# Kernel tuning notes

Measured on AMD Instinct MI355X. Metric: run time of the kernel, lower is better.

The kernel has to match this reference:

```python
import jax, jax.numpy as jnp
import numpy as np

N_NODE = 10000
E = 320000
E_LINK = 1280000
D = 128            # emb_input_dim = n_factors*delta_d = hid_dim
EDGE_FEAT = 24     # 2 + ceil(64/3)
SEQ = 64
K = 3


def _propagate(x, src, dst, w, n_seg):
    # out[d] = sum_{e: dst[e]=d} w[e] * x[src[e]]  (sparse matvec via gather-scatter)
    return jax.ops.segment_sum(w[:, None] * x[src], dst, num_segments=n_seg)


def setup_inputs() -> dict:
    key = jax.random.key(0)
    ks = jax.random.split(key, 16)
    inp = {
        "h_entity": jax.random.normal(ks[0], (SEQ, N_NODE, D), dtype=jnp.float32),
        "x_link": jax.random.normal(ks[1], (E, EDGE_FEAT), dtype=jnp.float32),
        "edge_weight_link": jax.random.uniform(ks[2], (E_LINK,), dtype=jnp.float32),
        "edge_index_link": jax.random.randint(ks[3], (2, E_LINK), 0, E, dtype=jnp.int32),
        "edge_index": jax.random.randint(ks[4], (2, E), 0, N_NODE, dtype=jnp.int32),
    }
    s = 0.05
    inp.update({
        "W_start": jax.random.normal(ks[5], (EDGE_FEAT, D), dtype=jnp.float32) * s,
        "b_start": jnp.zeros((D,), jnp.float32),
        "W_hl": jax.random.normal(ks[6], (K, D, D), dtype=jnp.float32) * s,
        "b_hl": jnp.zeros((D,), jnp.float32),
        "W_ec": jax.random.normal(ks[7], (D, K * 2), dtype=jnp.float32) * s,
        "b_ec": jnp.zeros((K * 2,), jnp.float32),
        "W_t": jax.random.normal(ks[8], (SEQ, 1), dtype=jnp.float32) * s,
        "b_t": jnp.zeros((1,), jnp.float32),
        "W_gcn": jax.random.normal(ks[9], (K, D, D), dtype=jnp.float32) * s,
        "b_gcn": jnp.zeros((D,), jnp.float32),
    })
    return inp


def reference(h_entity, x_link, edge_weight_link, W_start, b_start, W_hl, b_hl,
              W_ec, b_ec, W_t, b_t, W_gcn, b_gcn, edge_index_link, edge_index):
    src_l, dst_l = edge_index_link[0], edge_index_link[1]
    src_n, dst_n = edge_index[0], edge_index[1]

    # start_mlp_edge
    h_link = x_link @ W_start + b_start                      # [E, D]

    # HodgeLaguerreConv, K=3: Laguerre polynomial recurrence on edge Laplacian L
    # Tx0 = x; Tx1 = (1 - L)x; Tx_{k+1} = ((2k+1-L)Tx_k - k Tx_{k-1})/(k+1)
    Tx0 = h_link
    out_e = Tx0 @ W_hl[0]
    Tx1 = Tx0 - _propagate(Tx0, src_l, dst_l, edge_weight_link, E)
    out_e = out_e + Tx1 @ W_hl[1]
    Tx2 = (3.0 * Tx1 - _propagate(Tx1, src_l, dst_l, edge_weight_link, E) - Tx0) * 0.5
    out_e = out_e + Tx2 @ W_hl[2] + b_hl                     # [E, D]

    # per-edge causal scores, K*2 columns
    score = out_e @ W_ec + b_ec                              # [E, 2K]

    # temporal projection: [T,N,D] -> permute -> [N,D,T] @ [T,1] -> [N,D]
    h_ent = jnp.einsum('tnd,t->nd', h_entity, W_t[:, 0]) + b_t[0]

    # K-hop GCN: hop-k edge weight = softmax over the (causal, non-causal) pair k
    w_k = jax.nn.softmax(score.reshape(E, K, 2), axis=-1)[..., 0]  # [E, K]
    h = h_ent
    out_n = jnp.zeros((N_NODE, D), dtype=h_ent.dtype)
    for k in range(K):
        h = _propagate(h, src_n, dst_n, w_k[:, k], N_NODE)
        out_n = out_n + h @ W_gcn[k]
    out_n = out_n + b_gcn
    return out_n
```

## Files before the change

### kernel.cpp

```cpp
#include <hip/hip_runtime.h>

#define N_NODE   10000
#define E_EDGE   320000
#define E_LINKN  1280000
#define DIM      128
#define EFEAT    24
#define SEQLEN   64

#define SCAN_CHUNK 4096
#define NB_L 79
#define NB_N 3

static const size_t OFF_DEGN  = 0;
static const size_t OFF_DEGL  = OFF_DEGN  + 10240*4;
static const size_t OFF_DONE  = OFF_DEGL  + (size_t)E_EDGE*4;
static const size_t ZERO_BYTES= OFF_DONE  + 256;
static const size_t OFF_CONST = ZERO_BYTES;
static const size_t OFF_V0    = OFF_CONST + 512*4;
static const size_t OFF_V12   = OFF_V0    + (size_t)E_EDGE*6*4;
static const size_t OFF_PW    = OFF_V12   + (size_t)E_EDGE*16*4;
static const size_t OFF_STARTN= OFF_PW    + (size_t)E_EDGE*16*4;
static const size_t OFF_SRCSN = OFF_STARTN+ 10304*4;
static const size_t OFF_POSN  = OFF_SRCSN + (size_t)E_EDGE*4;
static const size_t OFF_WKS4  = OFF_POSN  + (size_t)E_EDGE*4;
static const size_t OFF_STARTL= OFF_WKS4  + (size_t)E_EDGE*16;
static const size_t OFF_LSW   = OFF_STARTL+ ((size_t)E_EDGE+64)*4;
static const size_t OFF_HENT  = OFF_LSW   + (size_t)E_LINKN*8;
static const size_t OFF_HA    = OFF_HENT  + (size_t)N_NODE*DIM*4;
static const size_t OFF_HB    = OFF_HA    + (size_t)N_NODE*DIM*4;
static const size_t OFF_HC    = OFF_HB    + (size_t)N_NODE*DIM*4;
static const size_t OFF_PARTN = OFF_HC    + (size_t)N_NODE*DIM*4;
static const size_t OFF_PARTL = OFF_PARTN + 512*4;

__global__ void consts_kernel(const float* __restrict__ Wstart, const float* __restrict__ bstart,
                              const float* __restrict__ Whl,    const float* __restrict__ bhl,
                              const float* __restrict__ Wec,    const float* __restrict__ bec,
                              float* __restrict__ Ball, float* __restrict__ cvec,
                              int4* __restrict__ zreg) {
    __shared__ float M[128*129];
    __shared__ float sWec[768];
    __shared__ float A[768];
    int k = blockIdx.x;
    int t = threadIdx.x;

    for (int i = blockIdx.x*256 + t; i < (int)(ZERO_BYTES/16); i += 3*256)
        zreg[i] = make_int4(0, 0, 0, 0);

    for (int i = t; i < 768; i += 256) sWec[i] = Wec[i];

    const float* w0 = Whl;
    const float* w1 = Whl + 16384;
    const float* w2 = Whl + 32768;
    for (int idx = t; idx < 16384; idx += 256) {
        int r = idx >> 7, d = idx & 127;
        float m;
        if (k == 0)      m = w0[idx] + w1[idx] + w2[idx];
        else if (k == 1) m = -(w1[idx] + 2.f*w2[idx]);
        else             m = 0.5f * w2[idx];
        M[r*129 + d] = m;
    }
    __syncthreads();

    for (int idx = t; idx < 768; idx += 256) {
        int r = idx / 6, j = idx % 6;
        float s = 0.f;
        for (int d = 0; d < 128; d++) s += M[r*129 + d] * sWec[d*6 + j];
        A[idx] = s;
    }
    __syncthreads();

    if (t < 144) {
        int i = t / 6, j = t % 6;
        float s = 0.f;
        for (int r = 0; r < 128; r++) s += Wstart[i*128 + r] * A[r*6 + j];
        Ball[i*18 + k*6 + j] = s;
    } else if (t < 150) {
        int j = t - 144;
        float s = 0.f;
        for (int r = 0; r < 128; r++) s += bstart[r] * A[r*6 + j];
        cvec[k*6 + j] = s;
    } else if (k == 0 && t >= 160 && t < 166) {
        int j = t - 160;
        float s = bec[j];
        for (int d = 0; d < 128; d++) s += bhl[d] * sWec[d*6 + j];
        cvec[18 + j] = s;
    }
}

__global__ void v_hist_kernel(const float* __restrict__ x, const float* __restrict__ Ball,
                              const int* __restrict__ dstl, const int* __restrict__ dstn,
                              float* __restrict__ V0, float* __restrict__ V12,
                              int* __restrict__ degl, int* __restrict__ degn) {
    int e = blockIdx.x * 256 + threadIdx.x;
    atomicAdd(degl + dstl[e], 1);

    if (blockIdx.x >= 1250) return;
    atomicAdd(degn + dstn[e], 1);

    __shared__ float sB[432];
    for (int i = threadIdx.x; i < 432; i += 256) sB[i] = Ball[i];
    __syncthreads();

    float xr[24];
    const float4* xp = (const float4*)(x + (size_t)e*24);
#pragma unroll
    for (int q = 0; q < 6; q++) {
        float4 v = xp[q];
        xr[4*q+0] = v.x; xr[4*q+1] = v.y; xr[4*q+2] = v.z; xr[4*q+3] = v.w;
    }
    float o[18];
#pragma unroll
    for (int j = 0; j < 18; j++) o[j] = 0.f;
#pragma unroll
    for (int i = 0; i < 24; i++) {
        float xv = xr[i];
#pragma unroll
        for (int j = 0; j < 18; j++) o[j] += xv * sB[i*18 + j];
    }
    float2* v0p = (float2*)(V0 + (size_t)e*6);
    v0p[0] = make_float2(o[0], o[1]);
    v0p[1] = make_float2(o[2], o[3]);
    v0p[2] = make_float2(o[4], o[5]);
    float4* v12p = (float4*)(V12 + (size_t)e*16);
    v12p[0] = make_float4(o[6],  o[7],  o[8],  o[9]);
    v12p[1] = make_float4(o[10], o[11], o[12], o[13]);
    v12p[2] = make_float4(o[14], o[15], o[16], o[17]);
}

__global__ void partial_scanp_kernel(const int* __restrict__ degl, const int* __restrict__ degn,
                                     int* __restrict__ partl, int* __restrict__ partn,
                                     int* __restrict__ done,
                                     int* __restrict__ startl, int* __restrict__ startn) {
    __shared__ int red[256];
    __shared__ int lastflag;
    int b = blockIdx.x, t = threadIdx.x;

    const int* deg; int n, base; int* part;
    if (b < NB_L) { deg = degl; n = E_EDGE;  base = b*SCAN_CHUNK;          part = partl + b; }
    else          { deg = degn; n = N_NODE;  base = (b-NB_L)*SCAN_CHUNK;   part = partn + (b-NB_L); }

    int s = 0;
    for (int i = t; i < SCAN_CHUNK; i += 256) {
        int idx = base + i;
        if (idx < n) s += deg[idx];
    }
    red[t] = s;
    __syncthreads();
    for (int off = 128; off > 0; off >>= 1) {
        if (t < off) red[t] += red[t + off];
        __syncthreads();
    }
    if (t == 0) {
        *part = red[0];
        __threadfence();
        lastflag = (atomicAdd(done, 1) == NB_L + NB_N - 1);
    }
    __syncthreads();
    if (!lastflag) return;
    __threadfence();

    {
        __shared__ int a[256];
        a[t] = (t < NB_L) ? partl[t] : 0;
        __syncthreads();
        for (int off = 1; off < 256; off <<= 1) {
            int v = (t >= off) ? a[t - off] : 0;
            __syncthreads();
            a[t] += v;
            __syncthreads();
        }
        partl[256 + t] = (t == 0) ? 0 : a[t - 1];
        if (t == 255) startl[E_EDGE] = a[NB_L - 1];
    }
    __syncthreads();
    {
        __shared__ int a2[256];
        a2[t] = (t < NB_N) ? partn[t] : 0;
        __syncthreads();
        for (int off = 1; off < 256; off <<= 1) {
            int v = (t >= off) ? a2[t - off] : 0;
            __syncthreads();
            a2[t] += v;
            __syncthreads();
        }
        partn[256 + t] = (t == 0) ? 0 : a2[t - 1];
        if (t == 255) startn[N_NODE] = a2[NB_N - 1];
    }
}

__global__ void scan_block_kernel(const int* __restrict__ degl, const int* __restrict__ degn,
                                  const int* __restrict__ partl, const int* __restrict__ partn,
                                  int* __restrict__ startl, int* __restrict__ startn) {
    __shared__ int s[SCAN_CHUNK];
    __shared__ int tsum[256];
    int b = blockIdx.x, t = threadIdx.x;

    const int* deg; const int* offs; int* start; int n, base;
    if (b < NB_L) { deg = degl; offs = partl + 256; start = startl; n = E_EDGE; base = b*SCAN_CHUNK; }
    else { deg = degn; offs = partn + 256; start = startn; n = N_NODE; base = (b-NB_L)*SCAN_CHUNK; b -= NB_L; }

    for (int i = t; i < SCAN_CHUNK; i += 256) {
        int idx = base + i;
        s[i] = (idx < n) ? deg[idx] : 0;
    }
    __syncthreads();
    int lo = t * 16;
    int mysum = 0;
#pragma unroll
    for (int j = 0; j < 16; j++) mysum += s[lo + j];
    tsum[t] = mysum;
    __syncthreads();
    for (int off = 1; off < 256; off <<= 1) {
        int v = (t >= off) ? tsum[t - off] : 0;
        __syncthreads();
        tsum[t] += v;
        __syncthreads();
    }
    int run = offs[b] + ((t == 0) ? 0 : tsum[t - 1]);
#pragma unroll
    for (int j = 0; j < 16; j++) {
        int v = s[lo + j];
        s[lo + j] = run;
        run += v;
    }
    __syncthreads();
    for (int i = t; i < SCAN_CHUNK; i += 256) {
        int idx = base + i;
        if (idx < n) start[idx] = s[i];
    }
}

__global__ void fill_both_kernel(const int* __restrict__ srcl, const int* __restrict__ dstl,
                                 const float* __restrict__ ewl,
                                 const int* __restrict__ srcn, const int* __restrict__ dstn,
                                 const int* __restrict__ startl, const int* __restrict__ startn,
                                 int* __restrict__ degl, int* __restrict__ degn,
                                 int2* __restrict__ lsw,
                                 int* __restrict__ srcs_srt, int* __restrict__ posn) {
    int e = blockIdx.x * 256 + threadIdx.x;
    {
        int d = dstl[e];
        int old = atomicSub(degl + d, 1);
        int p = startl[d] + old - 1;
        lsw[p] = make_int2(srcl[e], __float_as_int(ewl[e]));
    }
    if (blockIdx.x < 1250) {
        int d = dstn[e];
        int old = atomicSub(degn + d, 1);
        int p = startn[d] + old - 1;
        srcs_srt[p] = srcn[e];
        posn[e] = p;
    }
}

__global__ void prop1_gather(const float* __restrict__ V12, const int* __restrict__ startl,
                             const int2* __restrict__ lsw, float* __restrict__ PW) {
    int e = blockIdx.x * blockDim.x + threadIdx.x;
    if (e >= E_EDGE) return;
    int s0 = startl[e], s1 = startl[e + 1];
    float acc[12];
#pragma unroll
    for (int j = 0; j < 12; j++) acc[j] = 0.f;
    float ws = 0.f;
    int2 cur = make_int2(0, 0);
    if (s0 < s1) cur = lsw[s0];
    for (int j = s0; j < s1; j++) {
        int2 nxt = (j + 1 < s1) ? lsw[j + 1] : cur;
        float w = __int_as_float(cur.y);
        const float4* vp = (const float4*)(V12 + (size_t)cur.x*16);
#pragma unroll
        for (int q = 0; q < 3; q++) {
            float4 v = vp[q];
            acc[4*q+0] += w*v.x; acc[4*q+1] += w*v.y;
            acc[4*q+2] += w*v.z; acc[4*q+3] += w*v.w;
        }
        ws += w;
        cur = nxt;
    }
    float4* pw = (float4*)(PW + (size_t)e*16);
    pw[0] = make_float4(acc[0], acc[1], acc[2],  acc[3]);
    pw[1] = make_float4(acc[4], acc[5], acc[6],  acc[7]);
    pw[2] = make_float4(acc[8], acc[9], acc[10], acc[11]);
    pw[3] = make_float4(ws, 0.f, 0.f, 0.f);
}

__global__ void prop2score_kernel(const float* __restrict__ PW,
                                  const int* __restrict__ startl, const int2* __restrict__ lsw,
                                  const float* __restrict__ V0,
                                  const float* __restrict__ cvec, const int* __restrict__ posn,
                                  float4* __restrict__ wks4) {
    __shared__ float sc[24];
    if (threadIdx.x < 24) sc[threadIdx.x] = cvec[threadIdx.x];
    __syncthreads();
    int e = blockIdx.x * blockDim.x + threadIdx.x;
    if (e >= E_EDGE) return;
    int s0 = startl[e], s1 = startl[e + 1];
    float p2[6];
#pragma unroll
    for (int j = 0; j < 6; j++) p2[j] = 0.f;
    float ws2 = 0.f;
    int2 cur = make_int2(0, 0);
    if (s0 < s1) cur = lsw[s0];
    for (int j = s0; j < s1; j++) {
        int2 nxt = (j + 1 < s1) ? lsw[j + 1] : cur;
        float w = __int_as_float(cur.y);
        const float4* pv = (const float4*)(PW + (size_t)cur.x*16);
        float4 a = pv[1];
        float4 b = pv[2];
        float4 c = pv[3];
        p2[0] += w*a.z; p2[1] += w*a.w;
        p2[2] += w*b.x; p2[3] += w*b.y; p2[4] += w*b.z; p2[5] += w*b.w;
        ws2 += w * c.x;
        cur = nxt;
    }
    const float4* pe = (const float4*)(PW + (size_t)e*16);
    float4 q0 = pe[0];
    float4 q1 = pe[1];
    float  ws1 = pe[3].x;
    float pw6[6] = {q0.x, q0.y, q0.z, q0.w, q1.x, q1.y};
    const float2* v0p = (const float2*)(V0 + (size_t)e*6);
    float2 f0 = v0p[0], f1 = v0p[1], f2 = v0p[2];
    float v0r[6] = {f0.x, f0.y, f1.x, f1.y, f2.x, f2.y};
    float S[6];
#pragma unroll
    for (int j = 0; j < 6; j++)
        S[j] = v0r[j] + pw6[j] + p2[j]
             + ws1*sc[6 + j] + ws2*sc[12 + j] + sc[j] + sc[18 + j];
    int p = posn[e];
    float w0 = 1.f / (1.f + __expf(S[1] - S[0]));
    float w1 = 1.f / (1.f + __expf(S[3] - S[2]));
    float w2 = 1.f / (1.f + __expf(S[5] - S[4]));
    wks4[p] = make_float4(w0, w1, w2, 0.f);
}

__global__ void temporal_kernel(const float4* __restrict__ h_entity, const float* __restrict__ Wt,
                                const float* __restrict__ bt, float4* __restrict__ h_ent) {
    __shared__ float sw[SEQLEN];
    if (threadIdx.x < SEQLEN) sw[threadIdx.x] = Wt[threadIdx.x];
    __syncthreads();
    int i = blockIdx.x * blockDim.x + threadIdx.x;
    if (i >= N_NODE*DIM/4) return;
    float b = bt[0];
    float4 acc = make_float4(b, b, b, b);
#pragma unroll 8
    for (int t = 0; t < SEQLEN; t++) {
        float4 v = h_entity[(size_t)t * (N_NODE*DIM/4) + i];
        float w = sw[t];
        acc.x += w*v.x; acc.y += w*v.y; acc.z += w*v.z; acc.w += w*v.w;
    }
    h_ent[i] = acc;
}

__global__ void prop_hop(const float* __restrict__ h_cur, float* __restrict__ h_next,
                         const int* __restrict__ startn, const int* __restrict__ srcs_srt,
                         const float4* __restrict__ wks4, int k) {
    int half = threadIdx.x >> 7;
    int tid  = threadIdx.x & 127;
    int node = blockIdx.x * 2 + half;
    int s0 = startn[node], s1 = startn[node + 1];
    float acc = 0.f;
    int sn = 0; float w = 0.f;
    if (s0 < s1) {
        sn = srcs_srt[s0];
        float4 wv = wks4[s0];
        w = (k == 0) ? wv.x : (k == 1) ? wv.y : wv.z;
    }
    for (int j = s0; j < s1; j++) {
        int sn_c = sn; float w_c = w;
        if (j + 1 < s1) {
            sn = srcs_srt[j + 1];
            float4 wv = wks4[j + 1];
            w = (k == 0) ? wv.x : (k == 1) ? wv.y : wv.z;
        }
        acc += w_c * h_cur[(size_t)sn_c*DIM + tid];
    }
    h_next[(size_t)node*DIM + tid] = acc;
}

__global__ void __launch_bounds__(256)
gemm_final(const float* __restrict__ h1, const float* __restrict__ h2,
           const float* __restrict__ h3, const float* __restrict__ Wgcn,
           const float* __restrict__ bgcn, float* __restrict__ out) {
    __shared__ float sG[128*128];
    __shared__ float sh[32*128];
    int t = threadIdx.x;
    int cg = t & 31, rg = t >> 5;
    int c0 = cg * 4, r0 = rg * 4;
    int rbase = blockIdx.x * 32;
    int nrows = N_NODE - rbase; if (nrows > 32) nrows = 32;

    float4 bb = *(const float4*)(bgcn + c0);
    float acc[4][4];
#pragma unroll
    for (int r = 0; r < 4; r++) {
        acc[r][0] = bb.x; acc[r][1] = bb.y; acc[r][2] = bb.z; acc[r][3] = bb.w;
    }

    const float* hs0[3] = {h1, h2, h3};
    for (int k = 0; k < 3; k++) {
        __syncthreads();
        const float4* gk = (const float4*)(Wgcn + (size_t)k*16384);
        float4* sg4 = (float4*)sG;
        for (int i = t; i < 4096; i += 256) sg4[i] = gk[i];
        const float4* hg = (const float4*)(hs0[k] + (size_t)rbase*128);
        float4* sh4 = (float4*)sh;
        for (int i = t; i < 1024; i += 256)
            sh4[i] = ((i >> 5) < nrows) ? hg[i] : make_float4(0.f, 0.f, 0.f, 0.f);
        __syncthreads();
#pragma unroll 2
        for (int d4 = 0; d4 < 32; d4++) {
            float4 g0 = *(const float4*)(sG + (d4*4 + 0)*128 + c0);
            float4 g1 = *(const float4*)(sG + (d4*4 + 1)*128 + c0);
            float4 g2 = *(const float4*)(sG + (d4*4 + 2)*128 + c0);
            float4 g3 = *(const float4*)(sG + (d4*4 + 3)*128 + c0);
#pragma unroll
            for (int r = 0; r < 4; r++) {
                float4 hv = *(const float4*)(sh + (r0 + r)*128 + d4*4);
                acc[r][0] += hv.x*g0.x; acc[r][1] += hv.x*g0.y; acc[r][2] += hv.x*g0.z; acc[r][3] += hv.x*g0.w;
                acc[r][0] += hv.y*g1.x; acc[r][1] += hv.y*g1.y; acc[r][2] += hv.y*g1.z; acc[r][3] += hv.y*g1.w;
                acc[r][0] += hv.z*g2.x; acc[r][1] += hv.z*g2.y; acc[r][2] += hv.z*g2.z; acc[r][3] += hv.z*g2.w;
                acc[r][0] += hv.w*g3.x; acc[r][1] += hv.w*g3.y; acc[r][2] += hv.w*g3.z; acc[r][3] += hv.w*g3.w;
            }
        }
    }
#pragma unroll
    for (int r = 0; r < 4; r++) {
        if (r0 + r < nrows)
            *(float4*)(out + (size_t)(rbase + r0 + r)*128 + c0) =
                make_float4(acc[r][0], acc[r][1], acc[r][2], acc[r][3]);
    }
}

extern "C" void kernel_launch(void* const* d_in, const int* in_sizes, int n_in,
                              void* d_out, int out_size, void* d_ws, size_t ws_size,
                              hipStream_t stream) {
    const float* h_entity = (const float*)d_in[0];
    const float* x_link   = (const float*)d_in[1];
    const float* ewl      = (const float*)d_in[2];
    const int*   eil      = (const int*)d_in[3];
    const int*   ein      = (const int*)d_in[4];
    const float* Wstart   = (const float*)d_in[5];
    const float* bstart   = (const float*)d_in[6];
    const float* Whl      = (const float*)d_in[7];
    const float* bhl      = (const float*)d_in[8];
    const float* Wec      = (const float*)d_in[9];
    const float* bec      = (const float*)d_in[10];
    const float* Wt       = (const float*)d_in[11];
    const float* bt       = (const float*)d_in[12];
    const float* Wgcn     = (const float*)d_in[13];
    const float* bgcn     = (const float*)d_in[14];
    float* out = (float*)d_out;
    char*  ws  = (char*)d_ws;

    const int* srcl = eil;
    const int* dstl = eil + E_LINKN;
    const int* srcn = ein;
    const int* dstn = ein + E_EDGE;

    int*    degn  = (int*)   (ws + OFF_DEGN);
    int*    degl  = (int*)   (ws + OFF_DEGL);
    int*    done  = (int*)   (ws + OFF_DONE);
    float*  Ball  = (float*) (ws + OFF_CONST);
    float*  cvec  = Ball + 432;
    float*  V0    = (float*) (ws + OFF_V0);
    float*  V12   = (float*) (ws + OFF_V12);
    float*  PW    = (float*) (ws + OFF_PW);
    int*    startn= (int*)   (ws + OFF_STARTN);
    int*    srcsn = (int*)   (ws + OFF_SRCSN);
    int*    posn  = (int*)   (ws + OFF_POSN);
    float4* wks4  = (float4*)(ws + OFF_WKS4);
    int*    startl= (int*)   (ws + OFF_STARTL);
    int2*   lsw   = (int2*)  (ws + OFF_LSW);
    float*  h_ent = (float*) (ws + OFF_HENT);
    float*  h_a   = (float*) (ws + OFF_HA);
    float*  h_b   = (float*) (ws + OFF_HB);
    float*  h_c   = (float*) (ws + OFF_HC);
    int*    partn = (int*)   (ws + OFF_PARTN);
    int*    partl = (int*)   (ws + OFF_PARTL);

    consts_kernel<<<3, 256, 0, stream>>>(Wstart, bstart, Whl, bhl, Wec, bec,
                                         Ball, cvec, (int4*)ws);
    v_hist_kernel<<<E_LINKN/256, 256, 0, stream>>>(x_link, Ball, dstl, dstn,
                                                   V0, V12, degl, degn);
    partial_scanp_kernel<<<NB_L + NB_N, 256, 0, stream>>>(degl, degn, partl, partn,
                                                          done, startl, startn);
    scan_block_kernel<<<NB_L + NB_N, 256, 0, stream>>>(degl, degn, partl, partn,
                                                       startl, startn);
    fill_both_kernel<<<E_LINKN/256, 256, 0, stream>>>(srcl, dstl, ewl, srcn, dstn,
                                                      startl, startn, degl, degn,
                                                      lsw, srcsn, posn);
    prop1_gather<<<(E_EDGE + 255)/256, 256, 0, stream>>>(V12, startl, lsw, PW);
    prop2score_kernel<<<(E_EDGE + 255)/256, 256, 0, stream>>>(PW, startl, lsw, V0, cvec,
                                                              posn, wks4);
    temporal_kernel<<<(N_NODE*DIM/4 + 255)/256, 256, 0, stream>>>(
        (const float4*)h_entity, Wt, bt, (float4*)h_ent);
    prop_hop<<<N_NODE/2, 256, 0, stream>>>(h_ent, h_a, startn, srcsn, wks4, 0);
    prop_hop<<<N_NODE/2, 256, 0, stream>>>(h_a,   h_b, startn, srcsn, wks4, 1);
    prop_hop<<<N_NODE/2, 256, 0, stream>>>(h_b,   h_c, startn, srcsn, wks4, 2);
    gemm_final<<<(N_NODE + 31)/32, 256, 0, stream>>>(h_a, h_b, h_c, Wgcn, bgcn, out);
}
```

Baseline: 969.9 us.

## Split edge gathers across two lanes, shrink PW records, fuse temporal into hist

The temporal projection moves into extra blocks of the histogram/V kernel, so its bandwidth-heavy read of h_entity overlaps with the atomic histogram work and one launch is removed. Both Laguerre gather kernels now give each edge two lanes that walk alternate neighbors and combine results with a shuffle, which doubles parallelism on the latency-bound CSR loops. The 16-float PW record is split into two 8-float arrays (PWS for the self terms, PWG for the second-hop gather), so the second gather reads 32 bytes per neighbor instead of 48 scattered bytes. In exchange, half the lanes idle through the scoring tail, and load balance now depends on degree parity.

New measurement: 978.2 us. About the same (+0.9%).

```diff
diff --git a/kernel.cpp b/kernel.cpp
--- a/kernel.cpp
+++ b/kernel.cpp
@@ -18,8 +18,9 @@
 static const size_t OFF_CONST = ZERO_BYTES;
 static const size_t OFF_V0    = OFF_CONST + 512*4;
 static const size_t OFF_V12   = OFF_V0    + (size_t)E_EDGE*6*4;
-static const size_t OFF_PW    = OFF_V12   + (size_t)E_EDGE*16*4;
-static const size_t OFF_STARTN= OFF_PW    + (size_t)E_EDGE*16*4;
+static const size_t OFF_PWS   = OFF_V12   + (size_t)E_EDGE*16*4;
+static const size_t OFF_PWG   = OFF_PWS   + (size_t)E_EDGE*8*4;
+static const size_t OFF_STARTN= OFF_PWG   + (size_t)E_EDGE*8*4;
 static const size_t OFF_SRCSN = OFF_STARTN+ 10304*4;
 static const size_t OFF_POSN  = OFF_SRCSN + (size_t)E_EDGE*4;
 static const size_t OFF_WKS4  = OFF_POSN  + (size_t)E_EDGE*4;
@@ -87,14 +88,35 @@
     }
 }
 
-__global__ void v_hist_kernel(const float* __restrict__ x, const float* __restrict__ Ball,
-                              const int* __restrict__ dstl, const int* __restrict__ dstn,
-                              float* __restrict__ V0, float* __restrict__ V12,
-                              int* __restrict__ degl, int* __restrict__ degn) {
-    int e = blockIdx.x * 256 + threadIdx.x;
+__global__ void v_hist_temporal(const float* __restrict__ x, const float* __restrict__ Ball,
+                                const int* __restrict__ dstl, const int* __restrict__ dstn,
+                                float* __restrict__ V0, float* __restrict__ V12,
+                                int* __restrict__ degl, int* __restrict__ degn,
+                                const float4* __restrict__ h_entity,
+                                const float* __restrict__ Wt, const float* __restrict__ bt,
+                                float4* __restrict__ h_ent) {
+    int b = blockIdx.x;
+    if (b >= 5000) {
+        __shared__ float sw[SEQLEN];
+        if (threadIdx.x < SEQLEN) sw[threadIdx.x] = Wt[threadIdx.x];
+        __syncthreads();
+        int i = (b - 5000) * 256 + threadIdx.x;
+        float bb = bt[0];
+        float4 acc = make_float4(bb, bb, bb, bb);
+#pragma unroll 8
+        for (int t = 0; t < SEQLEN; t++) {
+            float4 v = h_entity[(size_t)t * (N_NODE*DIM/4) + i];
+            float w = sw[t];
+            acc.x += w*v.x; acc.y += w*v.y; acc.z += w*v.z; acc.w += w*v.w;
+        }
+        h_ent[i] = acc;
+        return;
+    }
+
+    int e = b * 256 + threadIdx.x;
     atomicAdd(degl + dstl[e], 1);
 
-    if (blockIdx.x >= 1250) return;
+    if (b >= 1250) return;
     atomicAdd(degn + dstn[e], 1);
 
     __shared__ float sB[432];
@@ -254,18 +276,20 @@
 }
 
 __global__ void prop1_gather(const float* __restrict__ V12, const int* __restrict__ startl,
-                             const int2* __restrict__ lsw, float* __restrict__ PW) {
-    int e = blockIdx.x * blockDim.x + threadIdx.x;
-    if (e >= E_EDGE) return;
+                             const int2* __restrict__ lsw,
+                             float* __restrict__ PWS, float* __restrict__ PWG) {
+    int gid = blockIdx.x * 256 + threadIdx.x;
+    int e = gid >> 1, half = gid & 1;
     int s0 = startl[e], s1 = startl[e + 1];
     float acc[12];
 #pragma unroll
     for (int j = 0; j < 12; j++) acc[j] = 0.f;
     float ws = 0.f;
+    int j = s0 + half;
     int2 cur = make_int2(0, 0);
-    if (s0 < s1) cur = lsw[s0];
-    for (int j = s0; j < s1; j++) {
-        int2 nxt = (j + 1 < s1) ? lsw[j + 1] : cur;
+    if (j < s1) cur = lsw[j];
+    for (; j < s1; j += 2) {
+        int2 nxt = (j + 2 < s1) ? lsw[j + 2] : cur;
         float w = __int_as_float(cur.y);
         const float4* vp = (const float4*)(V12 + (size_t)cur.x*16);
 #pragma unroll
@@ -277,14 +301,22 @@
         ws += w;
         cur = nxt;
     }
-    float4* pw = (float4*)(PW + (size_t)e*16);
-    pw[0] = make_float4(acc[0], acc[1], acc[2],  acc[3]);
-    pw[1] = make_float4(acc[4], acc[5], acc[6],  acc[7]);
-    pw[2] = make_float4(acc[8], acc[9], acc[10], acc[11]);
-    pw[3] = make_float4(ws, 0.f, 0.f, 0.f);
-}
-
-__global__ void prop2score_kernel(const float* __restrict__ PW,
+#pragma unroll
+    for (int q = 0; q < 12; q++) acc[q] += __shfl_xor(acc[q], 1);
+    ws += __shfl_xor(ws, 1);
+
+    if (half == 0) {
+        float4* p = (float4*)(PWS + (size_t)e*8);
+        p[0] = make_float4(acc[0], acc[1], acc[2], acc[3]);
+        p[1] = make_float4(acc[4], acc[5], ws, 0.f);
+    } else {
+        float4* p = (float4*)(PWG + (size_t)e*8);
+        p[0] = make_float4(acc[6], acc[7], acc[8], acc[9]);
+        p[1] = make_float4(acc[10], acc[11], ws, 0.f);
+    }
+}
+
+__global__ void prop2score_kernel(const float* __restrict__ PWS, const float* __restrict__ PWG,
                                   const int* __restrict__ startl, const int2* __restrict__ lsw,
                                   const float* __restrict__ V0,
                                   const float* __restrict__ cvec, const int* __restrict__ posn,
@@ -292,63 +324,49 @@
     __shared__ float sc[24];
     if (threadIdx.x < 24) sc[threadIdx.x] = cvec[threadIdx.x];
     __syncthreads();
-    int e = blockIdx.x * blockDim.x + threadIdx.x;
-    if (e >= E_EDGE) return;
+    int gid = blockIdx.x * 256 + threadIdx.x;
+    int e = gid >> 1, half = gid & 1;
     int s0 = startl[e], s1 = startl[e + 1];
     float p2[6];
 #pragma unroll
     for (int j = 0; j < 6; j++) p2[j] = 0.f;
     float ws2 = 0.f;
+    int j = s0 + half;
     int2 cur = make_int2(0, 0);
-    if (s0 < s1) cur = lsw[s0];
-    for (int j = s0; j < s1; j++) {
-        int2 nxt = (j + 1 < s1) ? lsw[j + 1] : cur;
+    if (j < s1) cur = lsw[j];
+    for (; j < s1; j += 2) {
+        int2 nxt = (j + 2 < s1) ? lsw[j + 2] : cur;
         float w = __int_as_float(cur.y);
-        const float4* pv = (const float4*)(PW + (size_t)cur.x*16);
-        float4 a = pv[1];
-        float4 b = pv[2];
-        float4 c = pv[3];
-        p2[0] += w*a.z; p2[1] += w*a.w;
-        p2[2] += w*b.x; p2[3] += w*b.y; p2[4] += w*b.z; p2[5] += w*b.w;
-        ws2 += w * c.x;
+        const float4* g = (const float4*)(PWG + (size_t)cur.x*8);
+        float4 g0 = g[0], g1 = g[1];
+        p2[0] += w*g0.x; p2[1] += w*g0.y; p2[2] += w*g0.z;
+        p2[3] += w*g0.w; p2[4] += w*g1.x; p2[5] += w*g1.y;
+        ws2 += w * g1.z;
         cur = nxt;
     }
-    const float4* pe = (const float4*)(PW + (size_t)e*16);
-    float4 q0 = pe[0];
-    float4 q1 = pe[1];
-    float  ws1 = pe[3].x;
+#pragma unroll
+    for (int q = 0; q < 6; q++) p2[q] += __shfl_xor(p2[q], 1);
+    ws2 += __shfl_xor(ws2, 1);
+    if (half) return;
+
+    const float4* ps = (const float4*)(PWS + (size_t)e*8);
+    float4 q0 = ps[0];
+    float4 q1 = ps[1];
     float pw6[6] = {q0.x, q0.y, q0.z, q0.w, q1.x, q1.y};
+    float ws1 = q1.z;
     const float2* v0p = (const float2*)(V0 + (size_t)e*6);
     float2 f0 = v0p[0], f1 = v0p[1], f2 = v0p[2];
     float v0r[6] = {f0.x, f0.y, f1.x, f1.y, f2.x, f2.y};
     float S[6];
 #pragma unroll
-    for (int j = 0; j < 6; j++)
-        S[j] = v0r[j] + pw6[j] + p2[j]
-             + ws1*sc[6 + j] + ws2*sc[12 + j] + sc[j] + sc[18 + j];
+    for (int jj = 0; jj < 6; jj++)
+        S[jj] = v0r[jj] + pw6[jj] + p2[jj]
+              + ws1*sc[6 + jj] + ws2*sc[12 + jj] + sc[jj] + sc[18 + jj];
     int p = posn[e];
     float w0 = 1.f / (1.f + __expf(S[1] - S[0]));
     float w1 = 1.f / (1.f + __expf(S[3] - S[2]));
     float w2 = 1.f / (1.f + __expf(S[5] - S[4]));
     wks4[p] = make_float4(w0, w1, w2, 0.f);
-}
-
-__global__ void temporal_kernel(const float4* __restrict__ h_entity, const float* __restrict__ Wt,
-                                const float* __restrict__ bt, float4* __restrict__ h_ent) {
-    __shared__ float sw[SEQLEN];
-    if (threadIdx.x < SEQLEN) sw[threadIdx.x] = Wt[threadIdx.x];
-    __syncthreads();
-    int i = blockIdx.x * blockDim.x + threadIdx.x;
-    if (i >= N_NODE*DIM/4) return;
-    float b = bt[0];
-    float4 acc = make_float4(b, b, b, b);
-#pragma unroll 8
-    for (int t = 0; t < SEQLEN; t++) {
-        float4 v = h_entity[(size_t)t * (N_NODE*DIM/4) + i];
-        float w = sw[t];
-        acc.x += w*v.x; acc.y += w*v.y; acc.z += w*v.z; acc.w += w*v.w;
-    }
-    h_ent[i] = acc;
 }
 
 __global__ void prop_hop(const float* __restrict__ h_cur, float* __restrict__ h_next,
@@ -464,7 +482,8 @@
     float*  cvec  = Ball + 432;
     float*  V0    = (float*) (ws + OFF_V0);
     float*  V12   = (float*) (ws + OFF_V12);
-    float*  PW    = (float*) (ws + OFF_PW);
+    float*  PWS   = (float*) (ws + OFF_PWS);
+    float*  PWG   = (float*) (ws + OFF_PWG);
     int*    startn= (int*)   (ws + OFF_STARTN);
     int*    srcsn = (int*)   (ws + OFF_SRCSN);
     int*    posn  = (int*)   (ws + OFF_POSN);
@@ -480,8 +499,10 @@
 
     consts_kernel<<<3, 256, 0, stream>>>(Wstart, bstart, Whl, bhl, Wec, bec,
                                          Ball, cvec, (int4*)ws);
-    v_hist_kernel<<<E_LINKN/256, 256, 0, stream>>>(x_link, Ball, dstl, dstn,
-                                                   V0, V12, degl, degn);
+    v_hist_temporal<<<6250, 256, 0, stream>>>(x_link, Ball, dstl, dstn,
+                                              V0, V12, degl, degn,
+                                              (const float4*)h_entity, Wt, bt,
+                                              (float4*)h_ent);
     partial_scanp_kernel<<<NB_L + NB_N, 256, 0, stream>>>(degl, degn, partl, partn,
                                                           done, startl, startn);
     scan_block_kernel<<<NB_L + NB_N, 256, 0, stream>>>(degl, degn, partl, partn,
@@ -489,11 +510,9 @@
     fill_both_kernel<<<E_LINKN/256, 256, 0, stream>>>(srcl, dstl, ewl, srcn, dstn,
                                                       startl, startn, degl, degn,
                                                       lsw, srcsn, posn);
-    prop1_gather<<<(E_EDGE + 255)/256, 256, 0, stream>>>(V12, startl, lsw, PW);
-    prop2score_kernel<<<(E_EDGE + 255)/256, 256, 0, stream>>>(PW, startl, lsw, V0, cvec,
-                                                              posn, wks4);
-    temporal_kernel<<<(N_NODE*DIM/4 + 255)/256, 256, 0, stream>>>(
-        (const float4*)h_entity, Wt, bt, (float4*)h_ent);
+    prop1_gather<<<2*E_EDGE/256, 256, 0, stream>>>(V12, startl, lsw, PWS, PWG);
+    prop2score_kernel<<<2*E_EDGE/256, 256, 0, stream>>>(PWS, PWG, startl, lsw, V0, cvec,
+                                                        posn, wks4);
     prop_hop<<<N_NODE/2, 256, 0, stream>>>(h_ent, h_a, startn, srcsn, wks4, 0);
     prop_hop<<<N_NODE/2, 256, 0, stream>>>(h_a,   h_b, startn, srcsn, wks4, 1);
     prop_hop<<<N_NODE/2, 256, 0, stream>>>(h_b,   h_c, startn, srcsn, wks4, 2);
```
